# Performance work log

Hardware: AMD Instinct MI355X
Metric: run time of the kernel (lower is better)

The kernel has to match this reference:

```python
import jax, jax.numpy as jnp
import numpy as np


def _chamfer(samp_pc, ref_pc):
    """Squared-L2 chamfer: returns (cost_p1_p2 [B,N], cost_p2_p1 [B,M]).

    samp_pc: [B, N, 3], ref_pc: [B, M, 3]
    """
    s2 = jnp.sum(samp_pc * samp_pc, axis=-1)  # [B, N]
    r2 = jnp.sum(ref_pc * ref_pc, axis=-1)    # [B, M]
    cross = jnp.einsum('bnd,bmd->bnm', samp_pc, ref_pc)  # [B, N, M]
    d2 = s2[:, :, None] + r2[:, None, :] - 2.0 * cross   # [B, N, M]
    d2 = jnp.maximum(d2, 0.0)  # numerical floor
    cost_p1_p2 = jnp.min(d2, axis=2)  # [B, N] nearest ref for each samp point
    cost_p2_p1 = jnp.min(d2, axis=1)  # [B, M] nearest samp for each ref point
    return cost_p1_p2, cost_p2_p1


def setup_inputs() -> dict:
    key = jax.random.key(0)
    k1, k2 = jax.random.split(key)
    B, N, M = 16, 2048, 8192
    ref_pc = jax.random.normal(k1, (B, M, 3), dtype=jnp.float32)
    samp_pc = jax.random.normal(k2, (B, N, 3), dtype=jnp.float32)
    return {"ref_pc": ref_pc, "samp_pc": samp_pc}


def reference(ref_pc, samp_pc):
    cost_p1_p2, cost_p2_p1 = _chamfer(samp_pc, ref_pc)
    cd_p = (jnp.sqrt(cost_p1_p2).mean(axis=1) + jnp.sqrt(cost_p2_p1).mean(axis=1)) / 2.0
    cd_t = cost_p1_p2.mean(axis=1) + cost_p2_p1.mean(axis=1)
    return (cd_p, cd_t)
```

## Files before the change

kernel.cpp:

```cpp
#include <hip/hip_runtime.h>
#include <math.h>

#define BB 16
#define NN 2048
#define MM 8192

#define BLK 256
#define R 4
#define G (BLK * R)
#define YS (MM / G)
#define QCH 32
#define ZS (NN / QCH)
#define QPH 16
#define PHASES (QCH / QPH)

typedef float v2f __attribute__((ext_vector_type(2)));

static __device__ __forceinline__ v2f v2_splat(float s) { v2f r; r.x = s; r.y = s; return r; }
static __device__ __forceinline__ v2f v2_fma(v2f a, v2f b, v2f c) {
#if __has_builtin(__builtin_elementwise_fma)
    return __builtin_elementwise_fma(a, b, c);
#else
    v2f r; r.x = fmaf(a.x, b.x, c.x); r.y = fmaf(a.y, b.y, c.y); return r;
#endif
}


__global__ void __launch_bounds__(BLK) prep_kernel(const float* __restrict__ ref,
                                                   const float* __restrict__ samp,
                                                   float4* __restrict__ ref4,
                                                   float4* __restrict__ samp_pk,
                                                   unsigned int* __restrict__ ws2) {
    int i = blockIdx.x * blockDim.x + threadIdx.x;
    const int PM = BB * MM;
    const int PPAIR = BB * NN / 2;
    if (i < PM) {
        float p1 = ref[(size_t)i * 3 + 0], p2 = ref[(size_t)i * 3 + 1], p3 = ref[(size_t)i * 3 + 2];
        float q = fmaf(p1, p1, fmaf(p2, p2, p3 * p3));
        ref4[i] = make_float4(-2.f * p1, -2.f * p2, -2.f * p3, q);
        ws2[i] = 0x7F800000u;
    } else if (i < PM + PPAIR) {
        int k = i - PM;
        const float* s0 = samp + (size_t)k * 6;
        float x0 = s0[0], y0 = s0[1], z0 = s0[2];
        float x1 = s0[3], y1 = s0[4], z1 = s0[5];
        float w0 = fmaf(x0, x0, fmaf(y0, y0, z0 * z0));
        float w1 = fmaf(x1, x1, fmaf(y1, y1, z1 * z1));
        samp_pk[(size_t)k * 2 + 0] = make_float4(x0, x1, y0, y1);
        samp_pk[(size_t)k * 2 + 1] = make_float4(z0, z1, w0, w1);
    }
}

__global__ void __launch_bounds__(BLK, 5) sweep_kernel(const float4* __restrict__ ref4,
                                                       const float4* __restrict__ samp_pk,
                                                       unsigned int* __restrict__ ws2,
                                                       float* __restrict__ ws1p) {
    __shared__ v2f tqbuf[(QPH / 2) * BLK];
    const int b = blockIdx.x;
    const int lane = threadIdx.x & 63;
    const int wv = threadIdx.x >> 6;
    const int refbase = blockIdx.y * G + wv * (64 * R);

    const float4* rp = ref4 + (size_t)b * MM + refbase;
    float px[R], py[R], pz[R], pp[R], mref[R];
#pragma unroll
    for (int r = 0; r < R; ++r) {
        float4 v = rp[r * 64 + lane];
        px[r] = v.x; py[r] = v.y; pz[r] = v.z; pp[r] = v.w;
        mref[r] = INFINITY;
    }

    const int q0 = blockIdx.z * QCH;
    const float4* qt = samp_pk + (size_t)b * NN + q0;
    float* w1 = ws1p + (size_t)blockIdx.y * (BB * NN) + (size_t)b * NN + q0;

    for (int ph = 0; ph < PHASES; ++ph) {
        const float4* qp = qt + ph * QPH;

#pragma unroll 4
        for (int j = 0; j < QPH / 2; ++j) {
            float4 a = qp[2 * j];
            float4 c = qp[2 * j + 1];
            v2f qx; qx.x = a.x; qx.y = a.y;
            v2f qy; qy.x = a.z; qy.y = a.w;
            v2f qz; qz.x = c.x; qz.y = c.y;
            v2f qw; qw.x = c.z; qw.y = c.w;
            v2f t[R];
#pragma unroll
            for (int r = 0; r < R; ++r) {
                v2f s = v2_fma(v2_splat(px[r]), qx, v2_splat(pp[r]));
                s = v2_fma(v2_splat(py[r]), qy, s);
                s = v2_fma(v2_splat(pz[r]), qz, s);
                t[r] = s + qw;
            }
#pragma unroll
            for (int r = 0; r < R; ++r)
                mref[r] = fminf(fminf(mref[r], t[r].x), t[r].y);
            v2f o;
            o.x = fminf(fminf(t[0].x, t[1].x), fminf(t[2].x, t[3].x));
            o.y = fminf(fminf(t[0].y, t[1].y), fminf(t[2].y, t[3].y));
            tqbuf[j * BLK + threadIdx.x] = o;
        }
        __syncthreads();

#pragma unroll
        for (int jj = 0; jj < (QPH / 2) / 4; ++jj) {
            const int jp = wv * ((QPH / 2) / 4) + jj;
            const v2f* s2 = tqbuf + jp * BLK;
            v2f v0 = s2[lane], v1 = s2[lane + 64], v2_ = s2[lane + 128], v3 = s2[lane + 192];
            float m0 = fminf(fminf(v0.x, v1.x), fminf(v2_.x, v3.x));
            float m1 = fminf(fminf(v0.y, v1.y), fminf(v2_.y, v3.y));
#pragma unroll
            for (int s = 32; s > 0; s >>= 1) {
                m0 = fminf(m0, __shfl_xor(m0, s));
                m1 = fminf(m1, __shfl_xor(m1, s));
            }
            if (lane == 0) {
                float2 st; st.x = m0; st.y = m1;
                *(float2*)(w1 + ph * QPH + 2 * jp) = st;
            }
        }
        __syncthreads();
    }

    unsigned int* w2 = ws2 + (size_t)b * MM + refbase;
#pragma unroll
    for (int r = 0; r < R; ++r)
        atomicMin(&w2[r * 64 + lane], __float_as_uint(fmaxf(mref[r], 0.f)));
}

#define BLKR 1024
__global__ void __launch_bounds__(BLKR) reduce_kernel(const float* __restrict__ ws1p,
                                                      const unsigned int* __restrict__ ws2,
                                                      float* __restrict__ out) {
    const int b = blockIdx.x;
    const int tid = threadIdx.x;

    float sd1 = 0.f, sr1 = 0.f;
    for (int i = tid; i < NN; i += BLKR) {
        float m = INFINITY;
#pragma unroll
        for (int y = 0; y < YS; ++y)
            m = fminf(m, ws1p[(size_t)y * (BB * NN) + (size_t)b * NN + i]);
        float v = fmaxf(m, 0.f);
        sd1 += v;
        sr1 += sqrtf(v);
    }
    float sd2 = 0.f, sr2 = 0.f;
    for (int i = tid; i < MM; i += BLKR) {
        float v = __uint_as_float(ws2[(size_t)b * MM + i]);
        sd2 += v;
        sr2 += sqrtf(v);
    }

    __shared__ float4 red[BLKR];
    red[tid] = make_float4(sd1, sr1, sd2, sr2);
    __syncthreads();
    for (int s = BLKR / 2; s > 0; s >>= 1) {
        if (tid < s) {
            red[tid].x += red[tid + s].x;
            red[tid].y += red[tid + s].y;
            red[tid].z += red[tid + s].z;
            red[tid].w += red[tid + s].w;
        }
        __syncthreads();
    }
    if (tid == 0) {
        float4 r = red[0];
        out[b]      = (r.y * (1.0f / NN) + r.w * (1.0f / MM)) * 0.5f;
        out[BB + b] = r.x * (1.0f / NN) + r.z * (1.0f / MM);
    }
}

extern "C" void kernel_launch(void* const* d_in, const int* in_sizes, int n_in,
                              void* d_out, int out_size, void* d_ws, size_t ws_size,
                              hipStream_t stream) {
    const float* ref  = (const float*)d_in[0];
    const float* samp = (const float*)d_in[1];
    float* out = (float*)d_out;

    float4* ref4    = (float4*)d_ws;
    float4* samp_pk = ref4 + (size_t)BB * MM;
    unsigned int* ws2 = (unsigned int*)(samp_pk + (size_t)BB * NN);
    float* ws1p = (float*)(ws2 + (size_t)BB * MM);

    const int P = BB * MM + BB * NN / 2;
    prep_kernel<<<(P + BLK - 1) / BLK, BLK, 0, stream>>>(ref, samp, ref4, samp_pk, ws2);

    dim3 gs(BB, YS, ZS);
    sweep_kernel<<<gs, BLK, 0, stream>>>(ref4, samp_pk, ws2, ws1p);

    reduce_kernel<<<BB, BLKR, 0, stream>>>(ws1p, ws2, out);
}
```

Before: 100.0 us.

## Fuse final reduction into sweep via last-block election and atomicMin row minima

```diff
diff --git a/kernel.cpp b/kernel.cpp
--- a/kernel.cpp
+++ b/kernel.cpp
@@ -13,6 +13,7 @@
 #define ZS (NN / QCH)
 #define QPH 16
 #define PHASES (QCH / QPH)
+#define BLOCKS_PER_BATCH (YS * ZS)
 
 typedef float v2f __attribute__((ext_vector_type(2)));
 
@@ -29,8 +30,7 @@
 __global__ void __launch_bounds__(BLK) prep_kernel(const float* __restrict__ ref,
                                                    const float* __restrict__ samp,
                                                    float4* __restrict__ ref4,
-                                                   float4* __restrict__ samp_pk,
-                                                   unsigned int* __restrict__ ws2) {
+                                                   float4* __restrict__ samp_pk) {
     int i = blockIdx.x * blockDim.x + threadIdx.x;
     const int PM = BB * MM;
     const int PPAIR = BB * NN / 2;
@@ -38,7 +38,6 @@
         float p1 = ref[(size_t)i * 3 + 0], p2 = ref[(size_t)i * 3 + 1], p3 = ref[(size_t)i * 3 + 2];
         float q = fmaf(p1, p1, fmaf(p2, p2, p3 * p3));
         ref4[i] = make_float4(-2.f * p1, -2.f * p2, -2.f * p3, q);
-        ws2[i] = 0x7F800000u;
     } else if (i < PM + PPAIR) {
         int k = i - PM;
         const float* s0 = samp + (size_t)k * 6;
@@ -54,8 +53,12 @@
 __global__ void __launch_bounds__(BLK, 5) sweep_kernel(const float4* __restrict__ ref4,
                                                        const float4* __restrict__ samp_pk,
                                                        unsigned int* __restrict__ ws2,
-                                                       float* __restrict__ ws1p) {
+                                                       unsigned int* __restrict__ ws1,
+                                                       unsigned int* __restrict__ counters,
+                                                       float* __restrict__ out) {
     __shared__ v2f tqbuf[(QPH / 2) * BLK];
+    __shared__ float4 red[BLK];
+    __shared__ unsigned int elect;
     const int b = blockIdx.x;
     const int lane = threadIdx.x & 63;
     const int wv = threadIdx.x >> 6;
@@ -72,7 +75,7 @@
 
     const int q0 = blockIdx.z * QCH;
     const float4* qt = samp_pk + (size_t)b * NN + q0;
-    float* w1 = ws1p + (size_t)blockIdx.y * (BB * NN) + (size_t)b * NN + q0;
+    unsigned int* w1 = ws1 + (size_t)b * NN + q0;
 
     for (int ph = 0; ph < PHASES; ++ph) {
         const float4* qp = qt + ph * QPH;
@@ -97,8 +100,8 @@
             for (int r = 0; r < R; ++r)
                 mref[r] = fminf(fminf(mref[r], t[r].x), t[r].y);
             v2f o;
-            o.x = fminf(fminf(t[0].x, t[1].x), fminf(t[2].x, t[3].x));
-            o.y = fminf(fminf(t[0].y, t[1].y), fminf(t[2].y, t[3].y));
+            o.x = fminf(fminf(fminf(t[0].x, t[1].x), t[2].x), t[3].x);
+            o.y = fminf(fminf(fminf(t[0].y, t[1].y), t[2].y), t[3].y);
             tqbuf[j * BLK + threadIdx.x] = o;
         }
         __syncthreads();
@@ -108,16 +111,16 @@
             const int jp = wv * ((QPH / 2) / 4) + jj;
             const v2f* s2 = tqbuf + jp * BLK;
             v2f v0 = s2[lane], v1 = s2[lane + 64], v2_ = s2[lane + 128], v3 = s2[lane + 192];
-            float m0 = fminf(fminf(v0.x, v1.x), fminf(v2_.x, v3.x));
-            float m1 = fminf(fminf(v0.y, v1.y), fminf(v2_.y, v3.y));
+            float m0 = fminf(fminf(fminf(v0.x, v1.x), v2_.x), v3.x);
+            float m1 = fminf(fminf(fminf(v0.y, v1.y), v2_.y), v3.y);
 #pragma unroll
             for (int s = 32; s > 0; s >>= 1) {
                 m0 = fminf(m0, __shfl_xor(m0, s));
                 m1 = fminf(m1, __shfl_xor(m1, s));
             }
             if (lane == 0) {
-                float2 st; st.x = m0; st.y = m1;
-                *(float2*)(w1 + ph * QPH + 2 * jp) = st;
+                atomicMin(&w1[ph * QPH + 2 * jp],     __float_as_uint(fmaxf(m0, 0.f)));
+                atomicMin(&w1[ph * QPH + 2 * jp + 1], __float_as_uint(fmaxf(m1, 0.f)));
             }
         }
         __syncthreads();
@@ -127,48 +130,44 @@
 #pragma unroll
     for (int r = 0; r < R; ++r)
         atomicMin(&w2[r * 64 + lane], __float_as_uint(fmaxf(mref[r], 0.f)));
-}
 
-#define BLKR 1024
-__global__ void __launch_bounds__(BLKR) reduce_kernel(const float* __restrict__ ws1p,
-                                                      const unsigned int* __restrict__ ws2,
-                                                      float* __restrict__ out) {
-    const int b = blockIdx.x;
-    const int tid = threadIdx.x;
-
-    float sd1 = 0.f, sr1 = 0.f;
-    for (int i = tid; i < NN; i += BLKR) {
-        float m = INFINITY;
-#pragma unroll
-        for (int y = 0; y < YS; ++y)
-            m = fminf(m, ws1p[(size_t)y * (BB * NN) + (size_t)b * NN + i]);
-        float v = fmaxf(m, 0.f);
-        sd1 += v;
-        sr1 += sqrtf(v);
+    __syncthreads();
+    if (threadIdx.x == 0) {
+        unsigned int old = atomicAdd(&counters[b], 1u);
+        elect = (old == BLOCKS_PER_BATCH - 1) ? 1u : 0u;
     }
-    float sd2 = 0.f, sr2 = 0.f;
-    for (int i = tid; i < MM; i += BLKR) {
-        float v = __uint_as_float(ws2[(size_t)b * MM + i]);
-        sd2 += v;
-        sr2 += sqrtf(v);
-    }
-
-    __shared__ float4 red[BLKR];
-    red[tid] = make_float4(sd1, sr1, sd2, sr2);
     __syncthreads();
-    for (int s = BLKR / 2; s > 0; s >>= 1) {
-        if (tid < s) {
-            red[tid].x += red[tid + s].x;
-            red[tid].y += red[tid + s].y;
-            red[tid].z += red[tid + s].z;
-            red[tid].w += red[tid + s].w;
+    if (elect != 0u) {
+        __threadfence();
+        const int tid = threadIdx.x;
+        float sd1 = 0.f, sr1 = 0.f;
+        for (int i = tid; i < NN; i += BLK) {
+            float v = __uint_as_float(ws1[(size_t)b * NN + i]);
+            sd1 += v;
+            sr1 += sqrtf(v);
         }
+        float sd2 = 0.f, sr2 = 0.f;
+        for (int i = tid; i < MM; i += BLK) {
+            float v = __uint_as_float(ws2[(size_t)b * MM + i]);
+            sd2 += v;
+            sr2 += sqrtf(v);
+        }
+        red[tid] = make_float4(sd1, sr1, sd2, sr2);
         __syncthreads();
-    }
-    if (tid == 0) {
-        float4 r = red[0];
-        out[b]      = (r.y * (1.0f / NN) + r.w * (1.0f / MM)) * 0.5f;
-        out[BB + b] = r.x * (1.0f / NN) + r.z * (1.0f / MM);
+        for (int s = BLK / 2; s > 0; s >>= 1) {
+            if (tid < s) {
+                red[tid].x += red[tid + s].x;
+                red[tid].y += red[tid + s].y;
+                red[tid].z += red[tid + s].z;
+                red[tid].w += red[tid + s].w;
+            }
+            __syncthreads();
+        }
+        if (tid == 0) {
+            float4 r = red[0];
+            out[b]      = (r.y * (1.0f / NN) + r.w * (1.0f / MM)) * 0.5f;
+            out[BB + b] = r.x * (1.0f / NN) + r.z * (1.0f / MM);
+        }
     }
 }
 
@@ -182,13 +181,15 @@
     float4* ref4    = (float4*)d_ws;
     float4* samp_pk = ref4 + (size_t)BB * MM;
     unsigned int* ws2 = (unsigned int*)(samp_pk + (size_t)BB * NN);
-    float* ws1p = (float*)(ws2 + (size_t)BB * MM);
+    unsigned int* ws1 = ws2 + (size_t)BB * MM;
+    unsigned int* counters = ws1 + (size_t)BB * NN;
+
+    hipMemsetAsync(ws2, 0x7F, (size_t)BB * (MM + NN) * sizeof(unsigned int), stream);
+    hipMemsetAsync(counters, 0, (size_t)BB * sizeof(unsigned int), stream);
 
     const int P = BB * MM + BB * NN / 2;
-    prep_kernel<<<(P + BLK - 1) / BLK, BLK, 0, stream>>>(ref, samp, ref4, samp_pk, ws2);
+    prep_kernel<<<(P + BLK - 1) / BLK, BLK, 0, stream>>>(ref, samp, ref4, samp_pk);
 
     dim3 gs(BB, YS, ZS);
-    sweep_kernel<<<gs, BLK, 0, stream>>>(ref4, samp_pk, ws2, ws1p);
-
-    reduce_kernel<<<BB, BLKR, 0, stream>>>(ws1p, ws2, out);
+    sweep_kernel<<<gs, BLK, 0, stream>>>(ref4, samp_pk, ws2, ws1, counters, out);
 }
```

New measurement: 179.0 us. 1.79x slower.
